# Kernel optimization log

Measured on AMD Instinct MI355X. Metric: run time of the kernel, lower is better.

The kernel has to match this reference:

```python
import jax, jax.numpy as jnp
import numpy as np

B, L, H, R = 8, 128, 768, 24


def setup_inputs() -> dict:
    key = jax.random.key(0)
    ks = jax.random.split(key, 12)
    s = 0.02  # init scale
    f32 = jnp.float32
    inp = {
        "embed_tokens": jax.random.normal(ks[0], (B, L, H), f32),
        "attention_mask": jnp.ones((B, L), f32),
        "target_rel": jax.random.randint(ks[1], (B,), 0, R),
        # relation-judgement head
        "W_hr": jax.random.normal(ks[2], (H, H // 2), f32) * s,
        "b_hr": jnp.zeros((H // 2,), f32),
        "W_rj": jax.random.normal(ks[3], (H // 2, R), f32) * s,
        "b_rj": jnp.zeros((R,), f32),
        # relation embedding
        "rel_emb": jax.random.normal(ks[4], (R, H), f32) * s,
        # correspondence matrix head (input is concat -> 2H)
        "W_corr": jax.random.normal(ks[5], (2 * H, H), f32) * s,
        "b_corr": jnp.zeros((H,), f32),
        "W_gc": jax.random.normal(ks[6], (H, 1), f32) * s,
        "b_gc": jnp.zeros((1,), f32),
        # subject tagging head (fusion_type='concat' -> 2H in, H hidden)
        "W_sh": jax.random.normal(ks[7], (2 * H, H), f32) * s,
        "b_sh": jnp.zeros((H,), f32),
        "W_st": jax.random.normal(ks[8], (H, 3), f32) * s,
        "b_st": jnp.zeros((3,), f32),
        # object tagging head
        "W_oh": jax.random.normal(ks[9], (2 * H, H), f32) * s,
        "b_oh": jnp.zeros((H,), f32),
        "W_ot": jax.random.normal(ks[10], (H, 3), f32) * s,
        "b_ot": jnp.zeros((3,), f32),
    }
    return inp


def reference(embed_tokens, attention_mask, target_rel,
              W_hr, b_hr, W_rj, b_rj, rel_emb,
              W_corr, b_corr, W_gc, b_gc,
              W_sh, b_sh, W_st, b_st,
              W_oh, b_oh, W_ot, b_ot):
    # ---- stage 1: masked mean-pool + relation judgement (dropout = identity at inference)
    masked = embed_tokens * attention_mask[:, :, None]            # [B,L,H]
    pool = jnp.sum(masked, axis=1) / jnp.sum(attention_mask, axis=1)[:, None]  # [B,H]
    rel_hidden = jax.nn.relu(pool @ W_hr + b_hr)                  # [B,H/2]
    stage1 = rel_hidden @ W_rj + b_rj                             # [B,R]

    # ---- correspondence matrix: concat[b,i,j] = [embed[b,j], embed[b,i]]
    # Decompose concat-linear: concat @ W_corr = embed_j @ W1 + embed_i @ W2
    W1, W2 = W_corr[:H_dim(embed_tokens)], W_corr[H_dim(embed_tokens):]
    A = embed_tokens @ W1                                         # [B,L,H] (j-index part)
    C = embed_tokens @ W2                                         # [B,L,H] (i-index part)
    corres_hidden = jax.nn.relu(A[:, None, :, :] + C[:, :, None, :] + b_corr)  # [B,L,L,H]
    pred_corres = corres_hidden @ W_gc + b_gc                     # [B,L,L,1]

    # ---- relation-fused tagging (mode == 'train')
    re = rel_emb[target_rel]                                      # [B,H]
    Bsz, Lsz, Hsz = embed_tokens.shape
    fusion = jnp.concatenate(
        [jnp.broadcast_to(re[:, None, :], (Bsz, Lsz, Hsz)), embed_tokens], axis=-1)  # [B,L,2H]
    subj = jax.nn.relu(fusion @ W_sh + b_sh) @ W_st + b_st        # [B,L,3]
    obj = jax.nn.relu(fusion @ W_oh + b_oh) @ W_ot + b_ot         # [B,L,3]

    return stage1, subj, obj, pred_corres


def H_dim(x):
    return x.shape[-1]
```

## Files before the change

kernel.cpp:

```cpp
#include <hip/hip_runtime.h>
#include <hip/hip_bf16.h>

#define BD   8
#define LD   128
#define HD   768
#define RD   24
#define H2D  384
#define NF   1536
#define WSZ  589824

typedef __attribute__((ext_vector_type(8))) short bf16x8;
typedef __attribute__((ext_vector_type(4))) float f32x4;

__device__ __forceinline__ short f2bf(float f) {
    __hip_bfloat16 h = __float2bfloat16(f);
    return *reinterpret_cast<short*>(&h);
}

__device__ __forceinline__ f32x4 vmax0(f32x4 v) {
    f32x4 r;
    r[0] = fmaxf(v[0], 0.f); r[1] = fmaxf(v[1], 0.f);
    r[2] = fmaxf(v[2], 0.f); r[3] = fmaxf(v[3], 0.f);
    return r;
}

__global__ __launch_bounds__(256) void prep_kernel(
        const float* __restrict__ embed, const float* __restrict__ mask,
        const float* __restrict__ rel_emb, const int* __restrict__ trel,
        const float* __restrict__ W_corr,
        const float* __restrict__ W_sh, const float* __restrict__ b_sh,
        const float* __restrict__ W_oh, const float* __restrict__ b_oh,
        const float* __restrict__ b_st, const float* __restrict__ b_ot,
        float* __restrict__ pool, float* __restrict__ biasrel,
        unsigned short* __restrict__ embedB, unsigned short* __restrict__ WT,
        float* __restrict__ out_subj, float* __restrict__ out_obj) {
    const int q = blockIdx.x, tid = threadIdx.x;

    if (q < 96) {
        const int b = q / 12, c = q % 12;
        __shared__ float mrow[LD];
        __shared__ float msum;
        __shared__ float part[4][64];
        if (tid < LD) mrow[tid] = mask[b * LD + tid];
        __syncthreads();
        if (tid == 0) {
            float s = 0.f;
            for (int l = 0; l < LD; ++l) s += mrow[l];
            msum = s;
        }
        __syncthreads();
        const int lc = tid >> 6, hh = tid & 63;
        const int h = c * 64 + hh;
        float acc = 0.f;
        const float* base = embed + ((size_t)b * LD + lc * 32) * HD + h;
#pragma unroll 8
        for (int i = 0; i < 32; ++i) acc += base[(size_t)i * HD] * mrow[lc * 32 + i];
        part[lc][hh] = acc;
        __syncthreads();
        if (lc == 0)
            pool[b * HD + h] = (part[0][hh] + part[1][hh] + part[2][hh] + part[3][hh]) / msum;
    } else if (q < 120) {
        const int c = q - 96;
        __shared__ float reAll[8][HD];
        __shared__ float part[4][8][64];
        for (int u = tid; u < 8 * HD; u += 256) {
            const int b = u / HD, k = u - b * HD;
            reAll[b][k] = rel_emb[(size_t)trel[b] * HD + k];
        }
        if (c == 0) {
            for (int u = tid; u < 3 * LD * BD; u += 256) {
                const int b = u / (3 * LD), rem = u - b * (3 * LD);
                const int l = rem / 3, t = rem - 3 * l;
                out_subj[(b * LD + l) * 3 + t] = b_st[t];
                out_obj [(b * LD + l) * 3 + t] = b_ot[t];
            }
        }
        __syncthreads();
        const int kc = tid >> 6, nn = tid & 63;
        const int n = c * 64 + nn;
        const float* Wp; int col;
        if (n < HD) { Wp = W_sh; col = n; }
        else        { Wp = W_oh; col = n - HD; }
        float acc[8] = {};
        for (int i = 0; i < 192; ++i) {
            const int k = kc * 192 + i;
            const float w = Wp[(size_t)k * HD + col];
#pragma unroll
            for (int b = 0; b < 8; ++b) acc[b] += reAll[b][k] * w;
        }
#pragma unroll
        for (int b = 0; b < 8; ++b) part[kc][b][nn] = acc[b];
        __syncthreads();
        {
            const float bb = (n < HD) ? b_sh[col] : b_oh[col];
            const int b0 = kc, b1 = kc + 4;
            float s0 = part[0][b0][nn] + part[1][b0][nn] + part[2][b0][nn] + part[3][b0][nn];
            float s1 = part[0][b1][nn] + part[1][b1][nn] + part[2][b1][nn] + part[3][b1][nn];
            biasrel[b0 * NF + n] = s0 + bb;
            biasrel[b1 * NF + n] = s1 + bb;
        }
    } else if (q < 216) {
        const int base = (q - 120) * 8192;
#pragma unroll
        for (int it = 0; it < 4; ++it) {
            const int off = base + it * 2048 + tid * 8;
            float4 v0 = *(const float4*)&embed[off];
            float4 v1 = *(const float4*)&embed[off + 4];
            bf16x8 p;
            p[0] = f2bf(v0.x); p[1] = f2bf(v0.y); p[2] = f2bf(v0.z); p[3] = f2bf(v0.w);
            p[4] = f2bf(v1.x); p[5] = f2bf(v1.y); p[6] = f2bf(v1.z); p[7] = f2bf(v1.w);
            *(bf16x8*)&embedB[off] = p;
        }
    } else {
        const int qq = q - 216;
        const int w = qq / 144, t = qq % 144;
        const int kt = t / 12, nt = t % 12;
        const float* src = (w == 0) ? W_corr
                         : (w == 1) ? W_corr + WSZ
                         : (w == 2) ? W_sh + WSZ
                                    : W_oh + WSZ;
        unsigned short* dst = WT + (size_t)w * WSZ;
        __shared__ float tile[64 * 65];
        const int r = tid >> 2, c4 = (tid & 3) * 16;
#pragma unroll
        for (int i = 0; i < 4; ++i) {
            float4 v = *(const float4*)&src[(size_t)(kt * 64 + r) * HD + nt * 64 + c4 + i * 4];
            tile[r * 65 + c4 + i * 4 + 0] = v.x;
            tile[r * 65 + c4 + i * 4 + 1] = v.y;
            tile[r * 65 + c4 + i * 4 + 2] = v.z;
            tile[r * 65 + c4 + i * 4 + 3] = v.w;
        }
        __syncthreads();
        bf16x8 p0, p1;
#pragma unroll
        for (int j = 0; j < 8; ++j) {
            p0[j] = f2bf(tile[(c4 + j) * 65 + r]);
            p1[j] = f2bf(tile[(c4 + 8 + j) * 65 + r]);
        }
        unsigned short* o = dst + (size_t)(nt * 64 + r) * HD + kt * 64 + c4;
        *(bf16x8*)(o)     = p0;
        *(bf16x8*)(o + 8) = p1;
    }
}

__global__ __launch_bounds__(256) void biggemm(
        const unsigned short* __restrict__ embedB,
        const unsigned short* __restrict__ WT,
        const float* __restrict__ biasrel,
        const float* __restrict__ W_st, const float* __restrict__ W_ot,
        const float* __restrict__ pool,
        const float* __restrict__ W_hr, const float* __restrict__ b_hr,
        float* __restrict__ AC, float* __restrict__ out_subj,
        float* __restrict__ out_obj, float* __restrict__ rh) {
    const int tid = threadIdx.x;

    if (blockIdx.x >= 24) {
        const int b = blockIdx.y >> 1;
        const int c = (blockIdx.x - 24) * 2 + (blockIdx.y & 1);
        __shared__ float prow[HD];
        __shared__ float rpart[4][64];
        for (int k = tid; k < HD; k += 256) prow[k] = pool[b * HD + k];
        __syncthreads();
        const int kc = tid >> 6, nn = tid & 63;
        const int n = c * 64 + nn;
        float acc = 0.f;
#pragma unroll 8
        for (int i = 0; i < 192; ++i) {
            const int k = kc * 192 + i;
            acc += prow[k] * W_hr[(size_t)k * H2D + n];
        }
        rpart[kc][nn] = acc;
        __syncthreads();
        if (kc == 0)
            rh[b * H2D + n] = fmaxf(rpart[0][nn] + rpart[1][nn] + rpart[2][nn] + rpart[3][nn] + b_hr[n], 0.f);
        return;
    }

    __shared__ __align__(16) short As [64][76];
    __shared__ __align__(16) short Bs0[64][76];
    __shared__ __align__(16) short Bs1[64][76];
    __shared__ float partial[64][3];

    const int bn0 = blockIdx.x * 64;
    const int bm0 = blockIdx.y * 64;

    const unsigned short* W0 = (bn0 < HD) ? WT : WT + WSZ;
    const unsigned short* W1 = (bn0 < HD) ? WT + 2 * (size_t)WSZ : WT + 3 * (size_t)WSZ;
    const int col0 = (bn0 < HD) ? bn0 : bn0 - HD;

    if (tid < 192) partial[tid / 3][tid % 3] = 0.f;

    const int row = tid >> 2;
    const int kc8 = (tid & 3) * 8;

    const int lane = tid & 63;
    const int wv = tid >> 6;
    const int wm = (wv >> 1) * 32;
    const int wn = (wv & 1) * 32;
    const int fr = lane & 15;
    const int kq = (lane >> 4) * 8;
    const int mq = (lane >> 4) * 4;

    f32x4 c00 = {0.f,0.f,0.f,0.f}, c01 = c00, c10 = c00, c11 = c00;
    f32x4 h00 = c00, h01 = c00, h10 = c00, h11 = c00;

    for (int kt = 0; kt < 12; ++kt) {
        const int k0 = kt << 6;
        const size_t ea = (size_t)(bm0 + row) * HD + k0 + kc8;
        const size_t wa = (size_t)(col0 + row) * HD + k0 + kc8;
        bf16x8 av0 = *(const bf16x8*)&embedB[ea];
        bf16x8 av1 = *(const bf16x8*)&embedB[ea + 32];
        bf16x8 b0v0 = *(const bf16x8*)&W0[wa];
        bf16x8 b0v1 = *(const bf16x8*)&W0[wa + 32];
        bf16x8 b1v0 = *(const bf16x8*)&W1[wa];
        bf16x8 b1v1 = *(const bf16x8*)&W1[wa + 32];

        __syncthreads();
        *(bf16x8*)&As [row][kc8]      = av0;
        *(bf16x8*)&As [row][kc8 + 32] = av1;
        *(bf16x8*)&Bs0[row][kc8]      = b0v0;
        *(bf16x8*)&Bs0[row][kc8 + 32] = b0v1;
        *(bf16x8*)&Bs1[row][kc8]      = b1v0;
        *(bf16x8*)&Bs1[row][kc8 + 32] = b1v1;
        __syncthreads();

#pragma unroll
        for (int kk = 0; kk < 2; ++kk) {
            const int kx = kq + kk * 32;
            bf16x8 a0 = *(bf16x8*)&As[wm + fr][kx];
            bf16x8 a1 = *(bf16x8*)&As[wm + 16 + fr][kx];
            bf16x8 b0 = *(bf16x8*)&Bs0[wn + fr][kx];
            bf16x8 b1 = *(bf16x8*)&Bs0[wn + 16 + fr][kx];
            bf16x8 d0 = *(bf16x8*)&Bs1[wn + fr][kx];
            bf16x8 d1 = *(bf16x8*)&Bs1[wn + 16 + fr][kx];
            c00 = __builtin_amdgcn_mfma_f32_16x16x32_bf16(a0, b0, c00, 0, 0, 0);
            c01 = __builtin_amdgcn_mfma_f32_16x16x32_bf16(a0, b1, c01, 0, 0, 0);
            c10 = __builtin_amdgcn_mfma_f32_16x16x32_bf16(a1, b0, c10, 0, 0, 0);
            c11 = __builtin_amdgcn_mfma_f32_16x16x32_bf16(a1, b1, c11, 0, 0, 0);
            h00 = __builtin_amdgcn_mfma_f32_16x16x32_bf16(a0, d0, h00, 0, 0, 0);
            h01 = __builtin_amdgcn_mfma_f32_16x16x32_bf16(a0, d1, h01, 0, 0, 0);
            h10 = __builtin_amdgcn_mfma_f32_16x16x32_bf16(a1, d0, h10, 0, 0, 0);
            h11 = __builtin_amdgcn_mfma_f32_16x16x32_bf16(a1, d1, h11, 0, 0, 0);
        }
    }

#pragma unroll
    for (int i = 0; i < 2; ++i) {
#pragma unroll
        for (int j = 0; j < 2; ++j) {
            f32x4 a = (i == 0) ? (j == 0 ? c00 : c01) : (j == 0 ? c10 : c11);
            const int ncol = bn0 + wn + j * 16 + fr;
#pragma unroll
            for (int r = 0; r < 4; ++r) {
                const int mrow = bm0 + wm + i * 16 + mq + r;
                AC[(size_t)mrow * NF + ncol] = a[r];
            }
        }
    }

    {
        const float* brl = biasrel + (size_t)(bm0 / LD) * NF;
        const float* Wt = (bn0 < HD) ? W_st : W_ot;
        float* op = (bn0 < HD) ? out_subj : out_obj;
        float pt[8][3] = {};
#pragma unroll
        for (int j = 0; j < 2; ++j) {
            const int ncol = bn0 + wn + j * 16 + fr;
            const int ncl = (bn0 < HD) ? ncol : ncol - HD;
            const float wt0 = Wt[ncl * 3 + 0];
            const float wt1 = Wt[ncl * 3 + 1];
            const float wt2 = Wt[ncl * 3 + 2];
            const float bias = brl[ncol];
#pragma unroll
            for (int i = 0; i < 2; ++i) {
                f32x4 a = (i == 0) ? (j == 0 ? h00 : h01) : (j == 0 ? h10 : h11);
#pragma unroll
                for (int r = 0; r < 4; ++r) {
                    const float v = fmaxf(a[r] + bias, 0.f);
                    pt[i * 4 + r][0] += v * wt0;
                    pt[i * 4 + r][1] += v * wt1;
                    pt[i * 4 + r][2] += v * wt2;
                }
            }
        }
#pragma unroll
        for (int mask = 1; mask < 16; mask <<= 1) {
#pragma unroll
            for (int x = 0; x < 8; ++x)
#pragma unroll
                for (int t = 0; t < 3; ++t)
                    pt[x][t] += __shfl_xor(pt[x][t], mask, 64);
        }
        if (fr == 0) {
#pragma unroll
            for (int i = 0; i < 2; ++i)
#pragma unroll
                for (int r = 0; r < 4; ++r)
#pragma unroll
                    for (int t = 0; t < 3; ++t)
                        atomicAdd(&partial[wm + i * 16 + mq + r][t], pt[i * 4 + r][t]);
        }
        __syncthreads();
        if (tid < 192) {
            const int m = tid / 3, t = tid % 3;
            atomicAdd(&op[(size_t)(bm0 + m) * 3 + t], partial[m][t]);
        }
    }
}

__global__ __launch_bounds__(512) void corres_kernel(
        const float* __restrict__ AC,
        const float* __restrict__ b_corr, const float* __restrict__ W_gc,
        const float* __restrict__ b_gc,
        const float* __restrict__ rh,
        const float* __restrict__ W_rj, const float* __restrict__ b_rj,
        float* __restrict__ out, float* __restrict__ out_stage1) {
    const int b = blockIdx.y;
    const int tid = threadIdx.x;

    if (blockIdx.x == 32) {
        __shared__ float rl[H2D];
        __shared__ float spart[8][RD];
        if (tid < H2D) rl[tid] = rh[b * H2D + tid];
        __syncthreads();
        if (tid < 8 * RD) {
            const int n = tid % RD, kc = tid / RD;
            float acc = 0.f;
#pragma unroll 8
            for (int i = 0; i < 48; ++i) {
                const int k = kc * 48 + i;
                acc += rl[k] * W_rj[k * RD + n];
            }
            spart[kc][n] = acc;
        }
        __syncthreads();
        if (tid < RD) {
            float s = b_rj[tid];
#pragma unroll
            for (int q = 0; q < 8; ++q) s += spart[q][tid];
            out_stage1[b * RD + tid] = s;
        }
        return;
    }

    const int i0 = blockIdx.x * 4;
    const int lane = tid & 63;
    const int wave = tid >> 6;

    f32x4 wg[3], cb[4][3];
#pragma unroll
    for (int s = 0; s < 3; ++s) {
        const int h = s * 256 + lane * 4;
        f32x4 w  = *(const f32x4*)&W_gc[h];
        f32x4 bc = *(const f32x4*)&b_corr[h];
        wg[s] = w;
#pragma unroll
        for (int i = 0; i < 4; ++i) {
            f32x4 cv = *(const f32x4*)&AC[((size_t)(b * LD + i0 + i)) * NF + HD + h];
            cb[i][s] = cv + bc;
        }
    }
    const float bg = b_gc[0];

    f32x4 a[3];
    {
        const float* ar = AC + ((size_t)(b * LD + wave)) * NF;
#pragma unroll
        for (int s = 0; s < 3; ++s) a[s] = *(const f32x4*)&ar[s * 256 + lane * 4];
    }
    for (int j = wave; j < LD; j += 8) {
        f32x4 an[3];
        if (j + 8 < LD) {
            const float* ar = AC + ((size_t)(b * LD + j + 8)) * NF;
#pragma unroll
            for (int s = 0; s < 3; ++s) an[s] = *(const f32x4*)&ar[s * 256 + lane * 4];
        }
        f32x4 sv[4];
#pragma unroll
        for (int i = 0; i < 4; ++i) sv[i] = (f32x4){0.f, 0.f, 0.f, 0.f};
#pragma unroll
        for (int s = 0; s < 3; ++s) {
#pragma unroll
            for (int i = 0; i < 4; ++i)
                sv[i] += vmax0(a[s] + cb[i][s]) * wg[s];
        }
#pragma unroll
        for (int i = 0; i < 4; ++i) {
            float r = (sv[i][0] + sv[i][1]) + (sv[i][2] + sv[i][3]);
#pragma unroll
            for (int off = 32; off > 0; off >>= 1) r += __shfl_down(r, off, 64);
            if (lane == 0)
                out[((size_t)(b * LD + i0 + i)) * LD + j] = r + bg;
        }
#pragma unroll
        for (int s = 0; s < 3; ++s) a[s] = an[s];
    }
}

extern "C" void kernel_launch(void* const* d_in, const int* in_sizes, int n_in,
                              void* d_out, int out_size, void* d_ws, size_t ws_size,
                              hipStream_t stream) {
    const float* embed   = (const float*)d_in[0];
    const float* mask    = (const float*)d_in[1];
    const int*   trel    = (const int*)d_in[2];
    const float* W_hr    = (const float*)d_in[3];
    const float* b_hr    = (const float*)d_in[4];
    const float* W_rj    = (const float*)d_in[5];
    const float* b_rj    = (const float*)d_in[6];
    const float* rel_emb = (const float*)d_in[7];
    const float* W_corr  = (const float*)d_in[8];
    const float* b_corr  = (const float*)d_in[9];
    const float* W_gc    = (const float*)d_in[10];
    const float* b_gc    = (const float*)d_in[11];
    const float* W_sh    = (const float*)d_in[12];
    const float* b_sh    = (const float*)d_in[13];
    const float* W_st    = (const float*)d_in[14];
    const float* b_st    = (const float*)d_in[15];
    const float* W_oh    = (const float*)d_in[16];
    const float* b_oh    = (const float*)d_in[17];
    const float* W_ot    = (const float*)d_in[18];
    const float* b_ot    = (const float*)d_in[19];
    float* out = (float*)d_out;

    float* ws      = (float*)d_ws;
    float* AC      = ws;
    float* biasrel = ws + 1572864;
    float* rh      = ws + 1572864 + 12288;
    float* pool    = ws + 1572864 + 12288 + 3072;
    unsigned short* embedB = (unsigned short*)(ws + 1594368);
    unsigned short* WT     = (unsigned short*)(ws + 1594368 + 393216);

    float* out_stage1 = out;
    float* out_subj   = out + 192;
    float* out_obj    = out + 3264;
    float* out_corr   = out + 6336;

    prep_kernel<<<792, 256, 0, stream>>>(embed, mask, rel_emb, trel, W_corr,
                                         W_sh, b_sh, W_oh, b_oh, b_st, b_ot,
                                         pool, biasrel, embedB, WT,
                                         out_subj, out_obj);

    biggemm<<<dim3(27, 16), 256, 0, stream>>>(embedB, WT, biasrel, W_st, W_ot,
                                              pool, W_hr, b_hr,
                                              AC, out_subj, out_obj, rh);

    corres_kernel<<<dim3(33, BD), 512, 0, stream>>>(AC, b_corr, W_gc, b_gc,
                                                    rh, W_rj, b_rj, out_corr, out_stage1);
}
```

Before: 161.3 us.

## Compute correspondence pairwise relu-dot in packed fp16 with fdot2, prefetch GEMM tiles

Stores the A/C projections as packed fp16 pairs with b_corr folded in, which halves the intermediate traffic. The pairwise correspondence kernel now evaluates relu(a+c)·w with packed half adds and max plus fdot2 accumulation. Each block covers an 8x64 tile, the H dimension is split across waves, and partial sums are reduced with LDS atomics. The GEMM loop also prefetches the next k-tile's global loads into registers before the MFMA work. This trades precision, since the hidden sums are now fp16, for higher ALU throughput and less memory traffic.

```diff
diff --git a/kernel.cpp b/kernel.cpp
--- a/kernel.cpp
+++ b/kernel.cpp
@@ -11,17 +11,29 @@
 
 typedef __attribute__((ext_vector_type(8))) short bf16x8;
 typedef __attribute__((ext_vector_type(4))) float f32x4;
+typedef _Float16 f16x2 __attribute__((ext_vector_type(2)));
 
 __device__ __forceinline__ short f2bf(float f) {
     __hip_bfloat16 h = __float2bfloat16(f);
     return *reinterpret_cast<short*>(&h);
 }
 
-__device__ __forceinline__ f32x4 vmax0(f32x4 v) {
-    f32x4 r;
-    r[0] = fmaxf(v[0], 0.f); r[1] = fmaxf(v[1], 0.f);
-    r[2] = fmaxf(v[2], 0.f); r[3] = fmaxf(v[3], 0.f);
-    return r;
+__device__ __forceinline__ unsigned int packh2(float a, float b) {
+    f16x2 p;
+    p[0] = (_Float16)a;
+    p[1] = (_Float16)b;
+    return __builtin_bit_cast(unsigned int, p);
+}
+
+__device__ __forceinline__ void dstep(float& acc, unsigned int cu, f16x2 a, f16x2 w) {
+    f16x2 t = a + __builtin_bit_cast(f16x2, cu);
+    f16x2 z = {(_Float16)0.f, (_Float16)0.f};
+    t = __builtin_elementwise_max(t, z);
+#if __has_builtin(__builtin_amdgcn_fdot2)
+    acc = __builtin_amdgcn_fdot2(t, w, acc, false);
+#else
+    acc += (float)t[0] * (float)w[0] + (float)t[1] * (float)w[1];
+#endif
 }
 
 __global__ __launch_bounds__(256) void prep_kernel(
@@ -31,8 +43,10 @@
         const float* __restrict__ W_sh, const float* __restrict__ b_sh,
         const float* __restrict__ W_oh, const float* __restrict__ b_oh,
         const float* __restrict__ b_st, const float* __restrict__ b_ot,
+        const float* __restrict__ W_gc,
         float* __restrict__ pool, float* __restrict__ biasrel,
         unsigned short* __restrict__ embedB, unsigned short* __restrict__ WT,
+        unsigned int* __restrict__ wg16,
         float* __restrict__ out_subj, float* __restrict__ out_obj) {
     const int q = blockIdx.x, tid = threadIdx.x;
 
@@ -111,7 +125,7 @@
             p[4] = f2bf(v1.x); p[5] = f2bf(v1.y); p[6] = f2bf(v1.z); p[7] = f2bf(v1.w);
             *(bf16x8*)&embedB[off] = p;
         }
-    } else {
+    } else if (q < 792) {
         const int qq = q - 216;
         const int w = qq / 144, t = qq % 144;
         const int kt = t / 12, nt = t % 12;
@@ -140,6 +154,11 @@
         unsigned short* o = dst + (size_t)(nt * 64 + r) * HD + kt * 64 + c4;
         *(bf16x8*)(o)     = p0;
         *(bf16x8*)(o + 8) = p1;
+    } else {
+        for (int u = tid; u < 384; u += 256) {
+            const int n = (u & 15) + (u >> 4) * 32;
+            wg16[u] = packh2(W_gc[n], W_gc[n + 16]);
+        }
     }
 }
 
@@ -150,7 +169,8 @@
         const float* __restrict__ W_st, const float* __restrict__ W_ot,
         const float* __restrict__ pool,
         const float* __restrict__ W_hr, const float* __restrict__ b_hr,
-        float* __restrict__ AC, float* __restrict__ out_subj,
+        const float* __restrict__ b_corr,
+        unsigned int* __restrict__ AC16, float* __restrict__ out_subj,
         float* __restrict__ out_obj, float* __restrict__ rh) {
     const int tid = threadIdx.x;
 
@@ -192,6 +212,8 @@
 
     const int row = tid >> 2;
     const int kc8 = (tid & 3) * 8;
+    const size_t eaBase = (size_t)(bm0 + row) * HD + kc8;
+    const size_t waBase = (size_t)(col0 + row) * HD + kc8;
 
     const int lane = tid & 63;
     const int wv = tid >> 6;
@@ -204,17 +226,17 @@
     f32x4 c00 = {0.f,0.f,0.f,0.f}, c01 = c00, c10 = c00, c11 = c00;
     f32x4 h00 = c00, h01 = c00, h10 = c00, h11 = c00;
 
+    bf16x8 av0, av1, b0v0, b0v1, b1v0, b1v1;
+    {
+        av0  = *(const bf16x8*)&embedB[eaBase];
+        av1  = *(const bf16x8*)&embedB[eaBase + 32];
+        b0v0 = *(const bf16x8*)&W0[waBase];
+        b0v1 = *(const bf16x8*)&W0[waBase + 32];
+        b1v0 = *(const bf16x8*)&W1[waBase];
+        b1v1 = *(const bf16x8*)&W1[waBase + 32];
+    }
+
     for (int kt = 0; kt < 12; ++kt) {
-        const int k0 = kt << 6;
-        const size_t ea = (size_t)(bm0 + row) * HD + k0 + kc8;
-        const size_t wa = (size_t)(col0 + row) * HD + k0 + kc8;
-        bf16x8 av0 = *(const bf16x8*)&embedB[ea];
-        bf16x8 av1 = *(const bf16x8*)&embedB[ea + 32];
-        bf16x8 b0v0 = *(const bf16x8*)&W0[wa];
-        bf16x8 b0v1 = *(const bf16x8*)&W0[wa + 32];
-        bf16x8 b1v0 = *(const bf16x8*)&W1[wa];
-        bf16x8 b1v1 = *(const bf16x8*)&W1[wa + 32];
-
         __syncthreads();
         *(bf16x8*)&As [row][kc8]      = av0;
         *(bf16x8*)&As [row][kc8 + 32] = av1;
@@ -223,6 +245,16 @@
         *(bf16x8*)&Bs1[row][kc8]      = b1v0;
         *(bf16x8*)&Bs1[row][kc8 + 32] = b1v1;
         __syncthreads();
+
+        if (kt < 11) {
+            const int k0 = (kt + 1) << 6;
+            av0  = *(const bf16x8*)&embedB[eaBase + k0];
+            av1  = *(const bf16x8*)&embedB[eaBase + k0 + 32];
+            b0v0 = *(const bf16x8*)&W0[waBase + k0];
+            b0v1 = *(const bf16x8*)&W0[waBase + k0 + 32];
+            b1v0 = *(const bf16x8*)&W1[waBase + k0];
+            b1v1 = *(const bf16x8*)&W1[waBase + k0 + 32];
+        }
 
 #pragma unroll
         for (int kk = 0; kk < 2; ++kk) {
@@ -244,16 +276,21 @@
         }
     }
 
-#pragma unroll
-    for (int i = 0; i < 2; ++i) {
-#pragma unroll
-        for (int j = 0; j < 2; ++j) {
-            f32x4 a = (i == 0) ? (j == 0 ? c00 : c01) : (j == 0 ? c10 : c11);
-            const int ncol = bn0 + wn + j * 16 + fr;
+    {
+        const int dbase = ((bn0 + wn) >> 5) << 4;
+        float bc0 = 0.f, bc1 = 0.f;
+        if (bn0 >= HD) {
+            bc0 = b_corr[bn0 + wn + fr - HD];
+            bc1 = b_corr[bn0 + wn + fr - HD + 16];
+        }
+#pragma unroll
+        for (int i = 0; i < 2; ++i) {
+            f32x4 a0 = (i == 0) ? c00 : c10;
+            f32x4 a1 = (i == 0) ? c01 : c11;
 #pragma unroll
             for (int r = 0; r < 4; ++r) {
                 const int mrow = bm0 + wm + i * 16 + mq + r;
-                AC[(size_t)mrow * NF + ncol] = a[r];
+                AC16[(size_t)mrow * 768 + dbase + fr] = packh2(a0[r] + bc0, a1[r] + bc1);
             }
         }
     }
@@ -309,8 +346,8 @@
 }
 
 __global__ __launch_bounds__(512) void corres_kernel(
-        const float* __restrict__ AC,
-        const float* __restrict__ b_corr, const float* __restrict__ W_gc,
+        const unsigned int* __restrict__ AC16,
+        const unsigned int* __restrict__ wg16,
         const float* __restrict__ b_gc,
         const float* __restrict__ rh,
         const float* __restrict__ W_rj, const float* __restrict__ b_rj,
@@ -343,57 +380,73 @@
         return;
     }
 
-    const int i0 = blockIdx.x * 4;
+    const int xt = blockIdx.x >> 1;
+    const int yg = blockIdx.x & 1;
+    const int X0 = xt * 8, Y0 = yg * 64;
     const int lane = tid & 63;
-    const int wave = tid >> 6;
-
-    f32x4 wg[3], cb[4][3];
-#pragma unroll
-    for (int s = 0; s < 3; ++s) {
-        const int h = s * 256 + lane * 4;
-        f32x4 w  = *(const f32x4*)&W_gc[h];
-        f32x4 bc = *(const f32x4*)&b_corr[h];
-        wg[s] = w;
-#pragma unroll
-        for (int i = 0; i < 4; ++i) {
-            f32x4 cv = *(const f32x4*)&AC[((size_t)(b * LD + i0 + i)) * NF + HD + h];
-            cb[i][s] = cv + bc;
-        }
-    }
-    const float bg = b_gc[0];
-
-    f32x4 a[3];
+    const int w8 = tid >> 6;
+
+    __shared__ float lds_out[8][64];
+    lds_out[w8][lane] = 0.f;
+
+    f16x2 av[48], wv[48];
     {
-        const float* ar = AC + ((size_t)(b * LD + wave)) * NF;
-#pragma unroll
-        for (int s = 0; s < 3; ++s) a[s] = *(const f32x4*)&ar[s * 256 + lane * 4];
-    }
-    for (int j = wave; j < LD; j += 8) {
-        f32x4 an[3];
-        if (j + 8 < LD) {
-            const float* ar = AC + ((size_t)(b * LD + j + 8)) * NF;
-#pragma unroll
-            for (int s = 0; s < 3; ++s) an[s] = *(const f32x4*)&ar[s * 256 + lane * 4];
-        }
-        f32x4 sv[4];
-#pragma unroll
-        for (int i = 0; i < 4; ++i) sv[i] = (f32x4){0.f, 0.f, 0.f, 0.f};
-#pragma unroll
-        for (int s = 0; s < 3; ++s) {
-#pragma unroll
-            for (int i = 0; i < 4; ++i)
-                sv[i] += vmax0(a[s] + cb[i][s]) * wg[s];
-        }
-#pragma unroll
-        for (int i = 0; i < 4; ++i) {
-            float r = (sv[i][0] + sv[i][1]) + (sv[i][2] + sv[i][3]);
-#pragma unroll
-            for (int off = 32; off > 0; off >>= 1) r += __shfl_down(r, off, 64);
-            if (lane == 0)
-                out[((size_t)(b * LD + i0 + i)) * LD + j] = r + bg;
-        }
-#pragma unroll
-        for (int s = 0; s < 3; ++s) a[s] = an[s];
+        const uint4* ap = (const uint4*)(AC16 + ((size_t)(b * LD + Y0 + lane)) * 768 + w8 * 48);
+        const uint4* wp = (const uint4*)(wg16 + w8 * 48);
+#pragma unroll
+        for (int k = 0; k < 12; ++k) {
+            const uint4 va = ap[k];
+            const uint4 vw = wp[k];
+            av[4*k+0] = __builtin_bit_cast(f16x2, va.x);
+            av[4*k+1] = __builtin_bit_cast(f16x2, va.y);
+            av[4*k+2] = __builtin_bit_cast(f16x2, va.z);
+            av[4*k+3] = __builtin_bit_cast(f16x2, va.w);
+            wv[4*k+0] = __builtin_bit_cast(f16x2, vw.x);
+            wv[4*k+1] = __builtin_bit_cast(f16x2, vw.y);
+            wv[4*k+2] = __builtin_bit_cast(f16x2, vw.z);
+            wv[4*k+3] = __builtin_bit_cast(f16x2, vw.w);
+        }
+    }
+    __syncthreads();
+
+    float acc[8];
+#pragma unroll
+    for (int x = 0; x < 8; ++x) acc[x] = 0.f;
+
+    const uint4* cbase = (const uint4*)(AC16 + ((size_t)(b * LD + X0)) * 768 + 384 + w8 * 48);
+    uint4 cc[12];
+#pragma unroll
+    for (int k = 0; k < 12; ++k) cc[k] = cbase[k];
+
+#pragma unroll
+    for (int x = 0; x < 8; ++x) {
+        uint4 nn[12];
+        if (x < 7) {
+            const uint4* np = cbase + (size_t)(x + 1) * 192;
+#pragma unroll
+            for (int k = 0; k < 12; ++k) nn[k] = np[k];
+        }
+        float a = acc[x];
+#pragma unroll
+        for (int k = 0; k < 12; ++k) {
+            dstep(a, cc[k].x, av[4*k+0], wv[4*k+0]);
+            dstep(a, cc[k].y, av[4*k+1], wv[4*k+1]);
+            dstep(a, cc[k].z, av[4*k+2], wv[4*k+2]);
+            dstep(a, cc[k].w, av[4*k+3], wv[4*k+3]);
+        }
+        acc[x] = a;
+        if (x < 7) {
+#pragma unroll
+            for (int k = 0; k < 12; ++k) cc[k] = nn[k];
+        }
+    }
+
+#pragma unroll
+    for (int x = 0; x < 8; ++x) atomicAdd(&lds_out[x][lane], acc[x]);
+    __syncthreads();
+    {
+        const int xo = tid >> 6, yo = tid & 63;
+        out[((size_t)(b * LD + X0 + xo)) * LD + Y0 + yo] = lds_out[xo][yo] + b_gc[0];
     }
 }
 
@@ -422,28 +475,29 @@
     const float* b_ot    = (const float*)d_in[19];
     float* out = (float*)d_out;
 
-    float* ws      = (float*)d_ws;
-    float* AC      = ws;
-    float* biasrel = ws + 1572864;
-    float* rh      = ws + 1572864 + 12288;
-    float* pool    = ws + 1572864 + 12288 + 3072;
-    unsigned short* embedB = (unsigned short*)(ws + 1594368);
-    unsigned short* WT     = (unsigned short*)(ws + 1594368 + 393216);
+    float* ws = (float*)d_ws;
+    unsigned int* AC16 = (unsigned int*)ws;
+    float* biasrel = ws + 786432;
+    float* rh      = ws + 786432 + 12288;
+    float* pool    = ws + 786432 + 12288 + 3072;
+    unsigned int* wg16 = (unsigned int*)(ws + 807936);
+    unsigned short* embedB = (unsigned short*)(ws + 808320);
+    unsigned short* WT     = (unsigned short*)(ws + 808320 + 393216);
 
     float* out_stage1 = out;
     float* out_subj   = out + 192;
     float* out_obj    = out + 3264;
     float* out_corr   = out + 6336;
 
-    prep_kernel<<<792, 256, 0, stream>>>(embed, mask, rel_emb, trel, W_corr,
-                                         W_sh, b_sh, W_oh, b_oh, b_st, b_ot,
-                                         pool, biasrel, embedB, WT,
+    prep_kernel<<<793, 256, 0, stream>>>(embed, mask, rel_emb, trel, W_corr,
+                                         W_sh, b_sh, W_oh, b_oh, b_st, b_ot, W_gc,
+                                         pool, biasrel, embedB, WT, wg16,
                                          out_subj, out_obj);
 
     biggemm<<<dim3(27, 16), 256, 0, stream>>>(embedB, WT, biasrel, W_st, W_ot,
-                                              pool, W_hr, b_hr,
-                                              AC, out_subj, out_obj, rh);
-
-    corres_kernel<<<dim3(33, BD), 512, 0, stream>>>(AC, b_corr, W_gc, b_gc,
+                                              pool, W_hr, b_hr, b_corr,
+                                              AC16, out_subj, out_obj, rh);
+
+    corres_kernel<<<dim3(33, BD), 512, 0, stream>>>(AC16, wg16, b_gc,
                                                     rh, W_rj, b_rj, out_corr, out_stage1);
 }
```

Result: faster. 153.8 us (-4.7%).
